# Performance work log

Hardware: AMD Instinct MI355X
Metric: run time of the kernel (lower is better)

The kernel has to match this reference:

```python
import jax, jax.numpy as jnp
import numpy as np

B, N, D, K = 64, 4096, 256, 32


def setup_inputs() -> dict:
    key = jax.random.key(0)
    kx, kc, ks = jax.random.split(key, 3)
    x = jax.random.normal(kx, (B, N, D), dtype=jnp.float32)
    # codebook: 'orthogonal' init approximated by normalized gaussian rows
    C = jax.random.normal(kc, (K, D), dtype=jnp.float32) / np.sqrt(D)
    # keras 'uniform' initializer: U(-0.05, 0.05)
    S = jax.random.uniform(ks, (K,), dtype=jnp.float32, minval=-0.05, maxval=0.05)
    return {"x": x, "C": C, "S": S}


def reference(x, C, S):
    """Deep-TEN encoding.
    r_ik = x_i - C_k ;  w = softmax_k(-S_k * ||r_ik||^2) ;  E_k = sum_i w_ik * r_ik.
    ||r||^2 expanded as ||x||^2 - 2 x.C + ||C||^2 to avoid the [B,N,K,D] residual;
    aggregation likewise split: E = einsum(w, x) - (sum_i w) * C.
    """
    x2 = jnp.sum(x * x, axis=-1, keepdims=True)          # [B,N,1]
    c2 = jnp.sum(C * C, axis=-1)                         # [K]
    xc = jnp.einsum('bnd,kd->bnk', x, C)                 # [B,N,K]
    dist = x2 - 2.0 * xc + c2                            # [B,N,K] = ||x_i - C_k||^2
    w = jax.nn.softmax(-S * dist, axis=-1)               # [B,N,K]
    # E_k = sum_i w_ik * (x_i - C_k)
    E = jnp.einsum('bnk,bnd->bkd', w, x) - jnp.sum(w, axis=1)[..., None] * C
    return E                                             # [B,K,D]
```

## Files before the change

kernel.cpp:

```cpp
#include <hip/hip_runtime.h>
#include <stdint.h>


#define NN 4096
#define DD 256
#define KK 32

typedef __attribute__((ext_vector_type(8))) short short8;
typedef __attribute__((ext_vector_type(4))) float float4v;

__device__ __forceinline__ unsigned short f2bf(float f) {
    unsigned u = __float_as_uint(f);
    return (unsigned short)((u + 0x7fffu + ((u >> 16) & 1u)) >> 16);
}
__device__ __forceinline__ unsigned pk2(float a, float b) {
    return (unsigned)f2bf(a) | ((unsigned)f2bf(b) << 16);
}
__device__ __forceinline__ short8 pack8(float4 a, float4 b) {
    short8 r;
    r[0] = (short)f2bf(a.x); r[1] = (short)f2bf(a.y);
    r[2] = (short)f2bf(a.z); r[3] = (short)f2bf(a.w);
    r[4] = (short)f2bf(b.x); r[5] = (short)f2bf(b.y);
    r[6] = (short)f2bf(b.z); r[7] = (short)f2bf(b.w);
    return r;
}
__device__ __forceinline__ int swx(int n) { return (n & 7) ^ ((n >> 2) & 6); }

#define DPP_ADD(v, ctrl) \
    ((v) + __int_as_float(__builtin_amdgcn_update_dpp( \
        0, __float_as_int(v), (ctrl), 0xf, 0xf, true)))

__launch_bounds__(256, 2)
__global__ void dten_kernel(const float* __restrict__ X,
                            const float* __restrict__ Cg,
                            const float* __restrict__ Sg,
                            float* __restrict__ out) {
    const int b     = blockIdx.y;
    const int chunk = blockIdx.x;
    const int tid   = threadIdx.x;
    const int lane  = tid & 63;
    const int wv    = tid >> 6;
    const int lk    = lane & 15;
    const int lq    = lane >> 4;

    __shared__ __align__(16) unsigned short xa[64 * 256];
    __shared__ __align__(16) unsigned short wt[32 * 64];
    __shared__ __align__(16) float x2s[64];
    __shared__ __align__(16) float c2p[8][32];
    __shared__ __align__(16) float c2s[32];
    __shared__ __align__(16) float wss[4][32];

    {
        int k = tid & 31, seg = tid >> 5;
        const float4* cr = (const float4*)(Cg + k * DD + seg * 32);
        float p = 0.f;
        #pragma unroll
        for (int i = 0; i < 8; ++i) {
            float4 u = cr[i];
            p += u.x*u.x + u.y*u.y + u.z*u.z + u.w*u.w;
        }
        c2p[seg][k] = p;
    }
    __syncthreads();
    if (tid < 32) {
        float s = 0.f;
        #pragma unroll
        for (int seg = 0; seg < 8; ++seg) s += c2p[seg][tid];
        c2s[tid] = s;
    }
    __syncthreads();

    float sk8[8], c2k8[8];
    #pragma unroll
    for (int kt = 0; kt < 2; ++kt)
        #pragma unroll
        for (int r = 0; r < 4; ++r) {
            int k = 16 * kt + 4 * lq + r;
            sk8[kt * 4 + r]  = Sg[k];
            c2k8[kt * 4 + r] = c2s[k];
        }

    short8 cfrag[2][8];
    #pragma unroll
    for (int kt = 0; kt < 2; ++kt) {
        const float* crow = Cg + (size_t)(16 * kt + lk) * DD + lq * 8;
        #pragma unroll
        for (int ch = 0; ch < 8; ++ch) {
            float4 u0 = *(const float4*)(crow + ch * 32);
            float4 u1 = *(const float4*)(crow + ch * 32 + 4);
            cfrag[kt][ch] = pack8(u0, u1);
        }
    }

    float4v eacc[2][4];
    #pragma unroll
    for (int i = 0; i < 2; ++i)
        #pragma unroll
        for (int j = 0; j < 4; ++j)
            eacc[i][j] = (float4v){0.f, 0.f, 0.f, 0.f};
    float wsr[8] = {0.f, 0.f, 0.f, 0.f, 0.f, 0.f, 0.f, 0.f};

    const int row_base = chunk * 256;
    const int nown = 16 * wv + lk;

    for (int t = 0; t < 4; ++t) {
        const int row0 = row_base + t * 64;
        __syncthreads();

        const float4* xt4 = (const float4*)(X + ((size_t)b * NN + row0) * DD);
        #pragma unroll
        for (int it = 0; it < 16; ++it) {
            int rl = wv * 16 + it;
            float4 v = xt4[rl * 64 + lane];
            float p = v.x*v.x + v.y*v.y + v.z*v.z + v.w*v.w;
            p = DPP_ADD(p, 0x111); p = DPP_ADD(p, 0x112);
            p = DPP_ADD(p, 0x114); p = DPP_ADD(p, 0x118);
            p = DPP_ADD(p, 0x142); p = DPP_ADD(p, 0x143);
            if (lane == 63) x2s[rl] = p;
            int cs = (lane >> 1) ^ swx(rl);
            uint2 w2 = make_uint2(pk2(v.x, v.y), pk2(v.z, v.w));
            *(uint2*)&xa[rl * 256 + cs * 8 + 4 * (lane & 1)] = w2;
        }

        float4v a0 = (float4v){0.f, 0.f, 0.f, 0.f};
        float4v a1 = (float4v){0.f, 0.f, 0.f, 0.f};
        {
            const int rowoff = nown * 256;
            const int s = swx(nown);
            #pragma unroll
            for (int ch = 0; ch < 8; ++ch) {
                int c = (4 * ch + lq) ^ s;
                short8 bf = *(const short8*)&xa[rowoff + c * 8];
                a0 = __builtin_amdgcn_mfma_f32_16x16x32_bf16(cfrag[0][ch], bf, a0, 0, 0, 0);
                a1 = __builtin_amdgcn_mfma_f32_16x16x32_bf16(cfrag[1][ch], bf, a1, 0, 0, 0);
            }
        }
        float x2n = x2s[nown];
        float aa[8];
        #pragma unroll
        for (int r = 0; r < 4; ++r) {
            aa[r]     = sk8[r]     * (2.f * a0[r] - x2n - c2k8[r]);
            aa[4 + r] = sk8[4 + r] * (2.f * a1[r] - x2n - c2k8[4 + r]);
        }
        float m = aa[0];
        #pragma unroll
        for (int i = 1; i < 8; ++i) m = fmaxf(m, aa[i]);
        m = fmaxf(m, __shfl_xor(m, 16));
        m = fmaxf(m, __shfl_xor(m, 32));
        float e[8], den = 0.f;
        #pragma unroll
        for (int i = 0; i < 8; ++i) { e[i] = __expf(aa[i] - m); den += e[i]; }
        den += __shfl_xor(den, 16);
        den += __shfl_xor(den, 32);
        float inv = __builtin_amdgcn_rcpf(den);
        {
            const int nhi = nown >> 3, nlo = nown & 7;
            #pragma unroll
            for (int i = 0; i < 8; ++i) {
                float w = e[i] * inv;
                wsr[i] += w;
                int k = 16 * (i >> 2) + 4 * lq + (i & 3);
                wt[k * 64 + ((nhi ^ (k & 7)) << 3) + nlo] = f2bf(w);
            }
        }
        __syncthreads();

        #pragma unroll
        for (int nc = 0; nc < 2; ++nc) {
            int nf = nc * 4 + lq;
            short8 af0 = *(const short8*)&wt[lk * 64 + ((nf ^ (lk & 7)) << 3)];
            short8 af1 = *(const short8*)&wt[(16 + lk) * 64 + ((nf ^ (lk & 7)) << 3)];
            #pragma unroll
            for (int dt = 0; dt < 4; ++dt) {
                int cb = 8 * wv + 2 * dt + (lk >> 3);
                short8 bf;
                #pragma unroll
                for (int j = 0; j < 8; ++j) {
                    int n2 = nc * 32 + lq * 8 + j;
                    bf[j] = (short)xa[n2 * 256 + ((cb ^ swx(n2)) << 3) + (lk & 7)];
                }
                eacc[0][dt] = __builtin_amdgcn_mfma_f32_16x16x32_bf16(af0, bf, eacc[0][dt], 0, 0, 0);
                eacc[1][dt] = __builtin_amdgcn_mfma_f32_16x16x32_bf16(af1, bf, eacc[1][dt], 0, 0, 0);
            }
        }
    }

    #pragma unroll
    for (int i = 0; i < 8; ++i) {
        wsr[i] += __shfl_xor(wsr[i], 1);
        wsr[i] += __shfl_xor(wsr[i], 2);
        wsr[i] += __shfl_xor(wsr[i], 4);
        wsr[i] += __shfl_xor(wsr[i], 8);
    }
    if (lk == 0) {
        #pragma unroll
        for (int i = 0; i < 8; ++i) {
            int k = 16 * (i >> 2) + 4 * lq + (i & 3);
            wss[wv][k] = wsr[i];
        }
    }
    __syncthreads();

    #pragma unroll
    for (int kt = 0; kt < 2; ++kt) {
        #pragma unroll
        for (int r = 0; r < 4; ++r) {
            int k = 16 * kt + 4 * lq + r;
            float wsk = wss[0][k] + wss[1][k] + wss[2][k] + wss[3][k];
            #pragma unroll
            for (int dt = 0; dt < 4; ++dt) {
                int d = 64 * wv + 16 * dt + lk;
                float val = eacc[kt][dt][r] - wsk * Cg[(size_t)k * DD + d];
                unsafeAtomicAdd(&out[((size_t)b * KK + k) * DD + d], val);
            }
        }
    }
}

extern "C" void kernel_launch(void* const* d_in, const int* in_sizes, int n_in,
                              void* d_out, int out_size, void* d_ws, size_t ws_size,
                              hipStream_t stream) {
    const float* X = (const float*)d_in[0];
    const float* C = (const float*)d_in[1];
    const float* S = (const float*)d_in[2];
    float* out = (float*)d_out;
    hipMemsetAsync(out, 0, (size_t)out_size * sizeof(float), stream);
    dim3 grid(16, 64);
    dten_kernel<<<grid, dim3(256), 0, stream>>>(X, C, S, out);
}
```

Baseline: 424.0 us.

## Add transposed bf16 X tile, truncating converts, and two-pass reduction replacing atomics

Stores a second, transposed and XOR-swizzled bf16 copy of each X tile in shared memory (pairs of rows packed per 32-bit word), so the aggregation MFMA B-operand can be gathered with four dword reads instead of eight scalar short reads. The bf16 conversion of X and of the weights now truncates via byte permute instead of round-to-nearest. The weight tile gets a padded row stride, replacing its swizzle. Final atomics plus memset are replaced by per-chunk partial writes to workspace and a separate reduce kernel. Shared memory use grows by 32KB, which may lower occupancy, truncation adds rounding error, and the extra kernel adds a launch and workspace traffic.

```diff
diff --git a/kernel.cpp b/kernel.cpp
--- a/kernel.cpp
+++ b/kernel.cpp
@@ -5,26 +5,28 @@
 #define NN 4096
 #define DD 256
 #define KK 32
+#define WTP 72
 
 typedef __attribute__((ext_vector_type(8))) short short8;
 typedef __attribute__((ext_vector_type(4))) float float4v;
 
-__device__ __forceinline__ unsigned short f2bf(float f) {
+__device__ __forceinline__ unsigned pk2t(float a, float b) {
+    return __builtin_amdgcn_perm(__float_as_uint(b), __float_as_uint(a), 0x07060302u);
+}
+__device__ __forceinline__ unsigned short f2bf_rne(float f) {
     unsigned u = __float_as_uint(f);
     return (unsigned short)((u + 0x7fffu + ((u >> 16) & 1u)) >> 16);
 }
-__device__ __forceinline__ unsigned pk2(float a, float b) {
-    return (unsigned)f2bf(a) | ((unsigned)f2bf(b) << 16);
-}
-__device__ __forceinline__ short8 pack8(float4 a, float4 b) {
+__device__ __forceinline__ short8 pack8_rne(float4 a, float4 b) {
     short8 r;
-    r[0] = (short)f2bf(a.x); r[1] = (short)f2bf(a.y);
-    r[2] = (short)f2bf(a.z); r[3] = (short)f2bf(a.w);
-    r[4] = (short)f2bf(b.x); r[5] = (short)f2bf(b.y);
-    r[6] = (short)f2bf(b.z); r[7] = (short)f2bf(b.w);
+    r[0] = (short)f2bf_rne(a.x); r[1] = (short)f2bf_rne(a.y);
+    r[2] = (short)f2bf_rne(a.z); r[3] = (short)f2bf_rne(a.w);
+    r[4] = (short)f2bf_rne(b.x); r[5] = (short)f2bf_rne(b.y);
+    r[6] = (short)f2bf_rne(b.z); r[7] = (short)f2bf_rne(b.w);
     return r;
 }
 __device__ __forceinline__ int swx(int n) { return (n & 7) ^ ((n >> 2) & 6); }
+__device__ __forceinline__ int gfun(int l) { return (l & 15) ^ (l >> 4); }
 
 #define DPP_ADD(v, ctrl) \
     ((v) + __int_as_float(__builtin_amdgcn_update_dpp( \
@@ -34,7 +36,7 @@
 __global__ void dten_kernel(const float* __restrict__ X,
                             const float* __restrict__ Cg,
                             const float* __restrict__ Sg,
-                            float* __restrict__ out) {
+                            float* __restrict__ ws) {
     const int b     = blockIdx.y;
     const int chunk = blockIdx.x;
     const int tid   = threadIdx.x;
@@ -44,7 +46,8 @@
     const int lq    = lane >> 4;
 
     __shared__ __align__(16) unsigned short xa[64 * 256];
-    __shared__ __align__(16) unsigned short wt[32 * 64];
+    __shared__ __align__(16) unsigned xt32[256 * 32];
+    __shared__ __align__(16) unsigned short wt[KK * WTP];
     __shared__ __align__(16) float x2s[64];
     __shared__ __align__(16) float c2p[8][32];
     __shared__ __align__(16) float c2s[32];
@@ -88,7 +91,7 @@
         for (int ch = 0; ch < 8; ++ch) {
             float4 u0 = *(const float4*)(crow + ch * 32);
             float4 u1 = *(const float4*)(crow + ch * 32 + 4);
-            cfrag[kt][ch] = pack8(u0, u1);
+            cfrag[kt][ch] = pack8_rne(u0, u1);
         }
     }
 
@@ -102,6 +105,7 @@
 
     const int row_base = chunk * 256;
     const int nown = 16 * wv + lk;
+    const int glane = gfun(lane);
 
     for (int t = 0; t < 4; ++t) {
         const int row0 = row_base + t * 64;
@@ -109,17 +113,35 @@
 
         const float4* xt4 = (const float4*)(X + ((size_t)b * NN + row0) * DD);
         #pragma unroll
-        for (int it = 0; it < 16; ++it) {
-            int rl = wv * 16 + it;
-            float4 v = xt4[rl * 64 + lane];
-            float p = v.x*v.x + v.y*v.y + v.z*v.z + v.w*v.w;
-            p = DPP_ADD(p, 0x111); p = DPP_ADD(p, 0x112);
-            p = DPP_ADD(p, 0x114); p = DPP_ADD(p, 0x118);
-            p = DPP_ADD(p, 0x142); p = DPP_ADD(p, 0x143);
-            if (lane == 63) x2s[rl] = p;
-            int cs = (lane >> 1) ^ swx(rl);
-            uint2 w2 = make_uint2(pk2(v.x, v.y), pk2(v.z, v.w));
-            *(uint2*)&xa[rl * 256 + cs * 8 + 4 * (lane & 1)] = w2;
+        for (int it = 0; it < 8; ++it) {
+            const int P  = 8 * wv + it;
+            const int r0 = 2 * P, r1 = r0 + 1;
+            float4 v0 = xt4[r0 * 64 + lane];
+            float4 v1 = xt4[r1 * 64 + lane];
+            float p0 = v0.x*v0.x + v0.y*v0.y + v0.z*v0.z + v0.w*v0.w;
+            float p1 = v1.x*v1.x + v1.y*v1.y + v1.z*v1.z + v1.w*v1.w;
+            p0 = DPP_ADD(p0, 0x111); p1 = DPP_ADD(p1, 0x111);
+            p0 = DPP_ADD(p0, 0x112); p1 = DPP_ADD(p1, 0x112);
+            p0 = DPP_ADD(p0, 0x114); p1 = DPP_ADD(p1, 0x114);
+            p0 = DPP_ADD(p0, 0x118); p1 = DPP_ADD(p1, 0x118);
+            p0 = DPP_ADD(p0, 0x142); p1 = DPP_ADD(p1, 0x142);
+            p0 = DPP_ADD(p0, 0x143); p1 = DPP_ADD(p1, 0x143);
+            if (lane == 63) { x2s[r0] = p0; x2s[r1] = p1; }
+            {
+                int cs0 = (lane >> 1) ^ swx(r0);
+                int cs1 = (lane >> 1) ^ swx(r1);
+                *(uint2*)&xa[r0 * 256 + cs0 * 8 + 4 * (lane & 1)] =
+                    make_uint2(pk2t(v0.x, v0.y), pk2t(v0.z, v0.w));
+                *(uint2*)&xa[r1 * 256 + cs1 * 8 + 4 * (lane & 1)] =
+                    make_uint2(pk2t(v1.x, v1.y), pk2t(v1.z, v1.w));
+            }
+            {
+                int base = lane * 128 + (P ^ glane);
+                xt32[base     ] = pk2t(v0.x, v1.x);
+                xt32[base + 32] = pk2t(v0.y, v1.y);
+                xt32[base + 64] = pk2t(v0.z, v1.z);
+                xt32[base + 96] = pk2t(v0.w, v1.w);
+            }
         }
 
         float4v a0 = (float4v){0.f, 0.f, 0.f, 0.f};
@@ -153,32 +175,30 @@
         den += __shfl_xor(den, 16);
         den += __shfl_xor(den, 32);
         float inv = __builtin_amdgcn_rcpf(den);
-        {
-            const int nhi = nown >> 3, nlo = nown & 7;
-            #pragma unroll
-            for (int i = 0; i < 8; ++i) {
-                float w = e[i] * inv;
-                wsr[i] += w;
-                int k = 16 * (i >> 2) + 4 * lq + (i & 3);
-                wt[k * 64 + ((nhi ^ (k & 7)) << 3) + nlo] = f2bf(w);
-            }
+        #pragma unroll
+        for (int i = 0; i < 8; ++i) {
+            float w = e[i] * inv;
+            wsr[i] += w;
+            int k = 16 * (i >> 2) + 4 * lq + (i & 3);
+            wt[k * WTP + nown] = (unsigned short)(__float_as_uint(w) >> 16);
         }
         __syncthreads();
 
         #pragma unroll
-        for (int nc = 0; nc < 2; ++nc) {
-            int nf = nc * 4 + lq;
-            short8 af0 = *(const short8*)&wt[lk * 64 + ((nf ^ (lk & 7)) << 3)];
-            short8 af1 = *(const short8*)&wt[(16 + lk) * 64 + ((nf ^ (lk & 7)) << 3)];
+        for (int s = 0; s < 2; ++s) {
+            short8 af0 = *(const short8*)&wt[lk * WTP + s * 32 + lq * 8];
+            short8 af1 = *(const short8*)&wt[(16 + lk) * WTP + s * 32 + lq * 8];
             #pragma unroll
             for (int dt = 0; dt < 4; ++dt) {
-                int cb = 8 * wv + 2 * dt + (lk >> 3);
+                const int d  = 64 * wv + 16 * dt + lk;
+                const int gl = gfun(d >> 2);
+                const int bb = d * 32 + s * 16;
                 short8 bf;
-                #pragma unroll
-                for (int j = 0; j < 8; ++j) {
-                    int n2 = nc * 32 + lq * 8 + j;
-                    bf[j] = (short)xa[n2 * 256 + ((cb ^ swx(n2)) << 3) + (lk & 7)];
-                }
+                unsigned* bw = (unsigned*)&bf;
+                bw[0] = xt32[bb + ((4 * lq + 0) ^ gl)];
+                bw[1] = xt32[bb + ((4 * lq + 1) ^ gl)];
+                bw[2] = xt32[bb + ((4 * lq + 2) ^ gl)];
+                bw[3] = xt32[bb + ((4 * lq + 3) ^ gl)];
                 eacc[0][dt] = __builtin_amdgcn_mfma_f32_16x16x32_bf16(af0, bf, eacc[0][dt], 0, 0, 0);
                 eacc[1][dt] = __builtin_amdgcn_mfma_f32_16x16x32_bf16(af1, bf, eacc[1][dt], 0, 0, 0);
             }
@@ -201,6 +221,7 @@
     }
     __syncthreads();
 
+    float* wsp = ws + (((size_t)b * 16 + chunk) * KK) * DD;
     #pragma unroll
     for (int kt = 0; kt < 2; ++kt) {
         #pragma unroll
@@ -210,11 +231,26 @@
             #pragma unroll
             for (int dt = 0; dt < 4; ++dt) {
                 int d = 64 * wv + 16 * dt + lk;
-                float val = eacc[kt][dt][r] - wsk * Cg[(size_t)k * DD + d];
-                unsafeAtomicAdd(&out[((size_t)b * KK + k) * DD + d], val);
-            }
-        }
-    }
+                wsp[k * DD + d] = eacc[kt][dt][r] - wsk * Cg[(size_t)k * DD + d];
+            }
+        }
+    }
+}
+
+__launch_bounds__(256)
+__global__ void reduce_kernel(const float* __restrict__ ws,
+                              float* __restrict__ out) {
+    const int o = blockIdx.x * 256 + threadIdx.x;
+    const int b = o >> 11;
+    const int rest = o & 2047;
+    const float4* w4 = (const float4*)ws + ((size_t)b * 16) * 2048 + rest;
+    float4 acc = make_float4(0.f, 0.f, 0.f, 0.f);
+    #pragma unroll
+    for (int c = 0; c < 16; ++c) {
+        float4 v = w4[(size_t)c * 2048];
+        acc.x += v.x; acc.y += v.y; acc.z += v.z; acc.w += v.w;
+    }
+    ((float4*)out)[o] = acc;
 }
 
 extern "C" void kernel_launch(void* const* d_in, const int* in_sizes, int n_in,
@@ -224,7 +260,8 @@
     const float* C = (const float*)d_in[1];
     const float* S = (const float*)d_in[2];
     float* out = (float*)d_out;
-    hipMemsetAsync(out, 0, (size_t)out_size * sizeof(float), stream);
+    float* ws  = (float*)d_ws;
     dim3 grid(16, 64);
-    dten_kernel<<<grid, dim3(256), 0, stream>>>(X, C, S, out);
-}
+    dten_kernel<<<grid, dim3(256), 0, stream>>>(X, C, S, ws);
+    reduce_kernel<<<dim3(512), dim3(256), 0, stream>>>(ws, out);
+}
```

New measurement: 386.6 us. 8.8% less time.
